# Optimization experiments

Measured on AMD Instinct MI355X. Metric: run time of the kernel, lower is better.

The kernel has to match this reference:

```python
import jax, jax.numpy as jnp
import numpy as np

N, K, D, E = 30000, 20, 128, 600000


def time_encode(t, w, b):
    # TGN TimeEncode: cos(Linear(1->D)(t)) ; t: [...], returns [..., D]
    return jnp.cos(t[..., None] * w + b)


def setup_inputs() -> dict:
    key = jax.random.key(0)
    ks = jax.random.split(key, 8)
    node_features = jax.random.normal(ks[0], (N, D), dtype=jnp.float32)
    timestamps = jax.random.uniform(ks[1], (N,), dtype=jnp.float32) * 1e4
    edge_features = jax.random.normal(ks[2], (E, D), dtype=jnp.float32)
    neighbors = jax.random.randint(ks[3], (N, K), 0, N, dtype=jnp.int32)
    edge_idxs = jax.random.randint(ks[4], (N, K), 0, E, dtype=jnp.int32)
    # edge interaction times precede the query timestamps (temporal neighbor sampling)
    edge_times = jax.random.uniform(ks[5], (N, K), dtype=jnp.float32) * timestamps[:, None]
    # TGN basis-frequency init for the time encoder
    time_w = (1.0 / 10.0 ** np.linspace(0, 9, D)).astype(np.float32)
    time_w = jnp.asarray(time_w)
    time_b = jnp.zeros((D,), dtype=jnp.float32)
    s1 = 1.0 / np.sqrt(3 * D)
    W1 = jax.random.normal(ks[6], (3 * D, D), dtype=jnp.float32) * s1
    b1 = jnp.zeros((D,), dtype=jnp.float32)
    W2 = jax.random.normal(ks[7], (3 * D, D), dtype=jnp.float32) * s1
    b2 = jnp.zeros((D,), dtype=jnp.float32)
    return {"node_features": node_features, "timestamps": timestamps,
            "edge_features": edge_features, "neighbors": neighbors,
            "edge_idxs": edge_idxs, "edge_times": edge_times,
            "time_w": time_w, "time_b": time_b,
            "W1": W1, "b1": b1, "W2": W2, "b2": b2}


def reference(node_features, timestamps, edge_features, neighbors, edge_idxs,
              edge_times, time_w, time_b, W1, b1, W2, b2):
    # layer-0 neighbor embeddings = raw node features gathered at neighbor ids
    neigh_feat = node_features[neighbors]                       # [N, K, D]
    # time deltas between query time and edge times, then cosine time encoding
    deltas = timestamps[:, None] - edge_times                   # [N, K]
    edge_time_emb = time_encode(deltas, time_w, time_b)         # [N, K, D]
    edge_feat = edge_features[edge_idxs]                        # [N, K, D]
    # GraphSumEmbedding.aggregate
    neighbors_features = jnp.concatenate(
        [neigh_feat, edge_time_emb, edge_feat], axis=-1)        # [N, K, 3D]
    h = neighbors_features @ W1 + b1                            # [N, K, D]
    neighbors_sum = jax.nn.relu(jnp.sum(h, axis=1))             # [N, D]
    src_time_emb = time_encode(jnp.zeros_like(timestamps), time_w, time_b)  # [N, D]
    source_features = jnp.concatenate([node_features, src_time_emb], axis=1)
    source_embedding = jnp.concatenate([neighbors_sum, source_features], axis=1)
    return source_embedding @ W2 + b2                           # [N, D]
```

## Files before the change

kernel.cpp:

```cpp
#include <hip/hip_runtime.h>
#include <math.h>

#define DD 128
#define KNB 20
#define K3 384

typedef unsigned short u16;
typedef __attribute__((ext_vector_type(8))) short short8;
typedef __attribute__((ext_vector_type(4))) float f32x4;

static __device__ __forceinline__ u16 f2bf(float x) {
    union { float f; unsigned u; } v; v.f = x;
    unsigned r = v.u + 0x7fffu + ((v.u >> 16) & 1u);
    return (u16)(r >> 16);
}

__global__ __launch_bounds__(DD) void const_kernel(
    const float* __restrict__ tb, const float* __restrict__ W2,
    const float* __restrict__ b2, float* __restrict__ cvec)
{
    int d = threadIdx.x;
    float acc = b2[d];
    #pragma unroll 8
    for (int i = 0; i < DD; ++i)
        acc = fmaf(cosf(tb[i]), W2[(size_t)(2 * DD + i) * DD + d], acc);
    cvec[d] = acc;
}

__global__ __launch_bounds__(256) void pack_w(
    const float* __restrict__ W1, const float* __restrict__ W2,
    u16* __restrict__ W1p, u16* __restrict__ W2p)
{
    int t = blockIdx.x * 256 + threadIdx.x;
    if (t < 6144) {
        int L = t & 63;
        int ct = (t >> 6) & 7;
        int kt = t >> 9;
        int n  = ct * 16 + (L & 15);
        int kb = kt * 32 + (L >> 4) * 8;
        u16* d = W1p + (size_t)t * 8;
        #pragma unroll
        for (int j = 0; j < 8; ++j) d[j] = f2bf(W1[(size_t)(kb + j) * DD + n]);
    } else if (t < 10240) {
        int u = t - 6144;
        int L = u & 63;
        int ct = (u >> 6) & 7;
        int kt = (u >> 9) & 3;
        int part = u >> 11;
        int n  = ct * 16 + (L & 15);
        int kb = part * DD + kt * 32 + (L >> 4) * 8;
        u16* d = W2p + (size_t)u * 8;
        #pragma unroll
        for (int j = 0; j < 8; ++j) d[j] = f2bf(W2[(size_t)(kb + j) * DD + n]);
    }
}

__global__ __launch_bounds__(DD) void agg_kernel(
    const float* __restrict__ nodef, const float* __restrict__ ts,
    const float* __restrict__ edgef, const int* __restrict__ neighbors,
    const int* __restrict__ edge_idxs, const float* __restrict__ edge_times,
    const float* __restrict__ tw, const float* __restrict__ tb,
    u16* __restrict__ aggbf, u16* __restrict__ nfbf)
{
    const int n = blockIdx.x;
    const int t = threadIdx.x;
    const float w = tw[t];
    const float b = tb[t];
    const float tn = ts[n];
    const int*   nb = neighbors  + (size_t)n * KNB;
    const int*   eg = edge_idxs  + (size_t)n * KNB;
    const float* et = edge_times + (size_t)n * KNB;

    float an = 0.f, at = 0.f, ae = 0.f;
    #pragma unroll
    for (int k = 0; k < KNB; ++k) {
        int ni = nb[k];
        int ei = eg[k];
        float dt = tn - et[k];
        an += nodef[(size_t)ni * DD + t];
        ae += edgef[(size_t)ei * DD + t];
        at += cosf(fmaf(dt, w, b));
    }
    u16* o = aggbf + (size_t)n * K3;
    o[t]          = f2bf(an);
    o[DD + t]     = f2bf(at);
    o[2 * DD + t] = f2bf(ae);
    nfbf[(size_t)n * DD + t] = f2bf(nodef[(size_t)n * DD + t]);
}

#define APITCH 392
#define HPITCH 136

__global__ __launch_bounds__(256) void fused_gemm(
    const u16* __restrict__ aggbf, const u16* __restrict__ nfbf,
    const u16* __restrict__ W1p, const u16* __restrict__ W2p,
    const float* __restrict__ b1, const float* __restrict__ cvec,
    float* __restrict__ out, int N)
{
    __shared__ __align__(16) u16 As[32 * APITCH];

    const int tid  = threadIdx.x;
    const int lane = tid & 63;
    const int wave = tid >> 6;
    const int row0 = blockIdx.x * 32;
    const int m0     = (wave & 1) * 16;
    const int ctbase = (wave >> 1) * 4;
    const int l15  = lane & 15;
    const int quad = lane >> 4;

    {
        const float4* ag4 = (const float4*)aggbf;
        #pragma unroll
        for (int i = 0; i < 6; ++i) {
            int idx = tid + i * 256;
            int r = idx / 48, c = idx - r * 48;
            float4 v = make_float4(0.f, 0.f, 0.f, 0.f);
            int row = row0 + r;
            if (row < N) v = ag4[(size_t)row * 48 + c];
            *(float4*)&As[r * APITCH + c * 8] = v;
        }
    }
    __syncthreads();

    f32x4 acc[4];
    #pragma unroll
    for (int c = 0; c < 4; ++c) acc[c] = (f32x4){0.f, 0.f, 0.f, 0.f};

    const short8* W1v = (const short8*)W1p;
    for (int kt = 0; kt < 12; ++kt) {
        short8 a = *(const short8*)&As[(m0 + l15) * APITCH + kt * 32 + quad * 8];
        #pragma unroll
        for (int c = 0; c < 4; ++c) {
            short8 b = W1v[(size_t)(kt * 8 + ctbase + c) * 64 + lane];
            acc[c] = __builtin_amdgcn_mfma_f32_16x16x32_bf16(a, b, acc[c], 0, 0, 0);
        }
    }
    __syncthreads();

    u16* Hs  = As;
    u16* NFs = As + 32 * HPITCH;
    #pragma unroll
    for (int c = 0; c < 4; ++c) {
        int col = (ctbase + c) * 16 + l15;
        float bb = (float)KNB * b1[col];
        #pragma unroll
        for (int r = 0; r < 4; ++r) {
            float h = acc[c][r] + bb;
            h = h > 0.f ? h : 0.f;
            Hs[(m0 + quad * 4 + r) * HPITCH + col] = f2bf(h);
        }
    }
    {
        const float4* nf4 = (const float4*)nfbf;
        #pragma unroll
        for (int i = 0; i < 2; ++i) {
            int idx = tid + i * 256;
            int r = idx >> 4, c = idx & 15;
            float4 v = make_float4(0.f, 0.f, 0.f, 0.f);
            int row = row0 + r;
            if (row < N) v = nf4[(size_t)row * 16 + c];
            *(float4*)&NFs[r * HPITCH + c * 8] = v;
        }
    }
    __syncthreads();

    f32x4 acc2[4];
    #pragma unroll
    for (int c = 0; c < 4; ++c) {
        float cv = cvec[(ctbase + c) * 16 + l15];
        acc2[c] = (f32x4){cv, cv, cv, cv};
    }
    const short8* W2v = (const short8*)W2p;
    for (int kt = 0; kt < 4; ++kt) {
        short8 aH = *(const short8*)&Hs[(m0 + l15) * HPITCH + kt * 32 + quad * 8];
        #pragma unroll
        for (int c = 0; c < 4; ++c) {
            short8 b = W2v[(size_t)(kt * 8 + ctbase + c) * 64 + lane];
            acc2[c] = __builtin_amdgcn_mfma_f32_16x16x32_bf16(aH, b, acc2[c], 0, 0, 0);
        }
        short8 aN = *(const short8*)&NFs[(m0 + l15) * HPITCH + kt * 32 + quad * 8];
        #pragma unroll
        for (int c = 0; c < 4; ++c) {
            short8 b = W2v[(size_t)((4 + kt) * 8 + ctbase + c) * 64 + lane];
            acc2[c] = __builtin_amdgcn_mfma_f32_16x16x32_bf16(aN, b, acc2[c], 0, 0, 0);
        }
    }

    #pragma unroll
    for (int c = 0; c < 4; ++c) {
        int col = (ctbase + c) * 16 + l15;
        #pragma unroll
        for (int r = 0; r < 4; ++r) {
            int row = row0 + m0 + quad * 4 + r;
            if (row < N) out[(size_t)row * DD + col] = acc2[c][r];
        }
    }
}

extern "C" void kernel_launch(void* const* d_in, const int* in_sizes, int n_in,
                              void* d_out, int out_size, void* d_ws, size_t ws_size,
                              hipStream_t stream)
{
    const float* nodef      = (const float*)d_in[0];
    const float* ts         = (const float*)d_in[1];
    const float* edgef      = (const float*)d_in[2];
    const int*   neighbors  = (const int*)d_in[3];
    const int*   edge_idxs  = (const int*)d_in[4];
    const float* edge_times = (const float*)d_in[5];
    const float* tw         = (const float*)d_in[6];
    const float* tb         = (const float*)d_in[7];
    const float* W1         = (const float*)d_in[8];
    const float* b1         = (const float*)d_in[9];
    const float* W2         = (const float*)d_in[10];
    const float* b2         = (const float*)d_in[11];
    float*       out        = (float*)d_out;

    const int N = in_sizes[1];

    u16*   aggbf = (u16*)d_ws;
    u16*   nfbf  = aggbf + (size_t)N * K3;
    u16*   W1p   = nfbf + (size_t)N * DD;
    u16*   W2p   = W1p + 12 * 8 * 64 * 8;
    float* cvec  = (float*)(W2p + 2 * 4 * 8 * 64 * 8);

    hipLaunchKernelGGL(const_kernel, dim3(1), dim3(DD), 0, stream,
                       tb, W2, b2, cvec);
    hipLaunchKernelGGL(pack_w, dim3(40), dim3(256), 0, stream,
                       W1, W2, W1p, W2p);
    hipLaunchKernelGGL(agg_kernel, dim3(N), dim3(DD), 0, stream,
                       nodef, ts, edgef, neighbors, edge_idxs, edge_times,
                       tw, tb, aggbf, nfbf);
    const int gb = (N + 31) / 32;
    hipLaunchKernelGGL(fused_gemm, dim3(gb), dim3(256), 0, stream,
                       aggbf, nfbf, W1p, W2p, b1, cvec, out, N);
}
```

Baseline: 520.8 us.

## Restructure aggregation kernel: 8 nodes per block, float4 gathers, hardware cosine

```diff
diff --git a/kernel.cpp b/kernel.cpp
--- a/kernel.cpp
+++ b/kernel.cpp
@@ -4,6 +4,7 @@
 #define DD 128
 #define KNB 20
 #define K3 384
+#define NPB 8
 
 typedef unsigned short u16;
 typedef __attribute__((ext_vector_type(8))) short short8;
@@ -13,6 +14,18 @@
     union { float f; unsigned u; } v; v.f = x;
     unsigned r = v.u + 0x7fffu + ((v.u >> 16) & 1u);
     return (u16)(r >> 16);
+}
+
+static __device__ __forceinline__ float fcos(float x) {
+    float r = x * 0.15915494309189535f;
+    r = __builtin_amdgcn_fractf(r);
+    return __builtin_amdgcn_cosf(r);
+}
+
+static __device__ __forceinline__ void st4bf(u16* p, float4 v) {
+    ushort4 s;
+    s.x = f2bf(v.x); s.y = f2bf(v.y); s.z = f2bf(v.z); s.w = f2bf(v.w);
+    *(ushort4*)p = s;
 }
 
 __global__ __launch_bounds__(DD) void const_kernel(
@@ -55,37 +68,73 @@
     }
 }
 
-__global__ __launch_bounds__(DD) void agg_kernel(
+__global__ __launch_bounds__(256) void agg_kernel(
     const float* __restrict__ nodef, const float* __restrict__ ts,
     const float* __restrict__ edgef, const int* __restrict__ neighbors,
     const int* __restrict__ edge_idxs, const float* __restrict__ edge_times,
     const float* __restrict__ tw, const float* __restrict__ tb,
-    u16* __restrict__ aggbf, u16* __restrict__ nfbf)
-{
-    const int n = blockIdx.x;
-    const int t = threadIdx.x;
-    const float w = tw[t];
-    const float b = tb[t];
-    const float tn = ts[n];
-    const int*   nb = neighbors  + (size_t)n * KNB;
-    const int*   eg = edge_idxs  + (size_t)n * KNB;
-    const float* et = edge_times + (size_t)n * KNB;
-
-    float an = 0.f, at = 0.f, ae = 0.f;
-    #pragma unroll
+    u16* __restrict__ aggbf, u16* __restrict__ nfbf, int N)
+{
+    __shared__ int   s_nb[NPB * KNB];
+    __shared__ int   s_eg[NPB * KNB];
+    __shared__ float s_dt[NPB * KNB];
+
+    const int tid = threadIdx.x;
+    const int n0  = blockIdx.x * NPB;
+
+    if (tid < NPB * KNB) {
+        int nsub = tid / KNB;
+        int k    = tid - nsub * KNB;
+        int nn   = n0 + nsub;
+        if (nn < N) {
+            s_nb[tid] = neighbors[(size_t)nn * KNB + k];
+            s_eg[tid] = edge_idxs[(size_t)nn * KNB + k];
+            s_dt[tid] = ts[nn] - edge_times[(size_t)nn * KNB + k];
+        } else {
+            s_nb[tid] = 0; s_eg[tid] = 0; s_dt[tid] = 0.f;
+        }
+    }
+    __syncthreads();
+
+    const int c    = tid & 31;
+    const int nsub = tid >> 5;
+    const int n    = n0 + nsub;
+
+    const float4* nf4 = (const float4*)nodef;
+    const float4* ef4 = (const float4*)edgef;
+    const float4  w4  = ((const float4*)tw)[c];
+    const float4  b4  = ((const float4*)tb)[c];
+
+    float4 an = make_float4(0.f, 0.f, 0.f, 0.f);
+    float4 ae = an, at = an;
+
+    const int*   nb  = s_nb + nsub * KNB;
+    const int*   eg  = s_eg + nsub * KNB;
+    const float* dtp = s_dt + nsub * KNB;
+
+    #pragma unroll 10
     for (int k = 0; k < KNB; ++k) {
-        int ni = nb[k];
-        int ei = eg[k];
-        float dt = tn - et[k];
-        an += nodef[(size_t)ni * DD + t];
-        ae += edgef[(size_t)ei * DD + t];
-        at += cosf(fmaf(dt, w, b));
-    }
-    u16* o = aggbf + (size_t)n * K3;
-    o[t]          = f2bf(an);
-    o[DD + t]     = f2bf(at);
-    o[2 * DD + t] = f2bf(ae);
-    nfbf[(size_t)n * DD + t] = f2bf(nodef[(size_t)n * DD + t]);
+        int   ni = nb[k];
+        int   ei = eg[k];
+        float dt = dtp[k];
+        float4 nv = nf4[(size_t)ni * 32 + c];
+        float4 ev = ef4[(size_t)ei * 32 + c];
+        an.x += nv.x; an.y += nv.y; an.z += nv.z; an.w += nv.w;
+        ae.x += ev.x; ae.y += ev.y; ae.z += ev.z; ae.w += ev.w;
+        at.x += fcos(fmaf(dt, w4.x, b4.x));
+        at.y += fcos(fmaf(dt, w4.y, b4.y));
+        at.z += fcos(fmaf(dt, w4.z, b4.z));
+        at.w += fcos(fmaf(dt, w4.w, b4.w));
+    }
+
+    if (n < N) {
+        u16* o = aggbf + (size_t)n * K3;
+        st4bf(o + 4 * c,           an);
+        st4bf(o + DD + 4 * c,      at);
+        st4bf(o + 2 * DD + 4 * c,  ae);
+        float4 sf = nf4[(size_t)n * 32 + c];
+        st4bf(nfbf + (size_t)n * DD + 4 * c, sf);
+    }
 }
 
 #define APITCH 392
@@ -227,10 +276,9 @@
                        tb, W2, b2, cvec);
     hipLaunchKernelGGL(pack_w, dim3(40), dim3(256), 0, stream,
                        W1, W2, W1p, W2p);
-    hipLaunchKernelGGL(agg_kernel, dim3(N), dim3(DD), 0, stream,
+    hipLaunchKernelGGL(agg_kernel, dim3((N + NPB - 1) / NPB), dim3(256), 0, stream,
                        nodef, ts, edgef, neighbors, edge_idxs, edge_times,
-                       tw, tb, aggbf, nfbf);
-    const int gb = (N + 31) / 32;
-    hipLaunchKernelGGL(fused_gemm, dim3(gb), dim3(256), 0, stream,
+                       tw, tb, aggbf, nfbf, N);
+    hipLaunchKernelGGL(fused_gemm, dim3((N + 31) / 32), dim3(256), 0, stream,
                        aggbf, nfbf, W1p, W2p, b1, cvec, out, N);
 }
```

Result: faster. 480.4 us (-7.8%).
